# Kernel tuning notes

Hardware: AMD Instinct MI355X
Metric: run time of the kernel (lower is better)

The kernel has to match this reference:

```python
import jax, jax.numpy as jnp
import numpy as np

N_NODES = 30000
N_EDGES = 150000
N_REL = 10
IN_DIM = 256
OUT_DIM = 256


def setup_inputs() -> dict:
    key = jax.random.key(0)
    ks = jax.random.split(key, 10)
    s = 1.0 / np.sqrt(IN_DIM)  # ~nn.Linear init scale
    return {
        "x": jax.random.normal(ks[0], (N_NODES, IN_DIM), jnp.float32),
        "W_self": jax.random.uniform(ks[1], (IN_DIM, OUT_DIM), jnp.float32, -s, s),
        "b_self": jax.random.uniform(ks[2], (OUT_DIM,), jnp.float32, -s, s),
        "W_fwd": jax.random.uniform(ks[3], (N_REL, IN_DIM, OUT_DIM), jnp.float32, -s, s),
        "b_fwd": jax.random.uniform(ks[4], (N_REL, OUT_DIM), jnp.float32, -s, s),
        "W_rev": jax.random.uniform(ks[5], (N_REL, IN_DIM, OUT_DIM), jnp.float32, -s, s),
        "b_rev": jax.random.uniform(ks[6], (N_REL, OUT_DIM), jnp.float32, -s, s),
        "dep_idx": jax.random.randint(ks[7], (N_EDGES,), 0, N_NODES, jnp.int32),
        "rel_idx": jax.random.randint(ks[8], (N_EDGES,), 0, N_REL, jnp.int32),
        "gov_idx": jax.random.randint(ks[9], (N_EDGES,), 0, N_NODES, jnp.int32),
    }


def reference(x, W_self, b_self, W_fwd, b_fwd, W_rev, b_rev, dep_idx, rel_idx, gov_idx):
    # self transform for every token: [N, out]
    out = x @ W_self + b_self
    # transform all nodes by every relation weight up-front: [R, N, out]
    H_fwd = jnp.einsum("ni,rio->rno", x, W_fwd) + b_fwd[:, None, :]
    H_rev = jnp.einsum("ni,rio->rno", x, W_rev) + b_rev[:, None, :]
    # per-edge gather: forward msg uses governor feature, reverse msg uses dependent
    msg_fwd = H_fwd[rel_idx, gov_idx]  # [E, out]
    msg_rev = H_rev[rel_idx, dep_idx]  # [E, out]
    # scatter-add: forward msg -> dependent, reverse msg -> governor
    out = out.at[dep_idx].add(msg_fwd)
    out = out.at[gov_idx].add(msg_rev)
    return out
```

## Files before the change

### kernel.cpp

```cpp
#include <hip/hip_runtime.h>

#define N_NODES 30000
#define N_EDGES 150000
#define N_REL 10
#define DIM 256

#define SORT_BLOCKS 120
#define SORT_CHUNK ((N_EDGES + SORT_BLOCKS - 1) / SORT_BLOCKS)

#define SCAN_CHUNK 256
#define SCAN_BLOCKS ((N_NODES + SCAN_CHUNK - 1) / SCAN_CHUNK)

#define PREP_XB 7500
#define PREP_WB 5376

typedef __attribute__((ext_vector_type(8))) short bf16x8;
typedef __attribute__((ext_vector_type(4))) float f32x4;

__device__ __forceinline__ unsigned short f2bf(float f) {
  union { float f; unsigned int u; } v; v.f = f;
  unsigned int u = v.u;
  unsigned int r = u + 0x7fffu + ((u >> 16) & 1u);
  return (unsigned short)(r >> 16);
}


__global__ void prep_hist_kernel(const float* __restrict__ x,
                                 const float* __restrict__ Wf,
                                 const float* __restrict__ Wr,
                                 const float* __restrict__ Ws,
                                 const int* __restrict__ rel,
                                 const int* __restrict__ dep,
                                 const int* __restrict__ gov,
                                 unsigned short* __restrict__ xbf,
                                 unsigned short* __restrict__ wt,
                                 int* __restrict__ block_counts,
                                 int* __restrict__ cnt) {
  int b = blockIdx.x;
  if (b < PREP_XB) {
    int idx = b * 256 + threadIdx.x;
    float4 v = reinterpret_cast<const float4*>(x)[idx];
    ushort4 o;
    o.x = f2bf(v.x); o.y = f2bf(v.y); o.z = f2bf(v.z); o.w = f2bf(v.w);
    reinterpret_cast<ushort4*>(xbf)[idx] = o;
  } else if (b < PREP_XB + PREP_WB) {
    int idx = (b - PREP_XB) * 256 + threadIdx.x;
    int bb = idx >> 16;
    int t = idx & 65535;
    int o = t >> 8, i = t & 255;
    const float* src = (bb < N_REL) ? (Wf + (size_t)bb * 65536)
                     : (bb < 2 * N_REL) ? (Wr + (size_t)(bb - N_REL) * 65536)
                     : Ws;
    wt[idx] = f2bf(src[i * 256 + o]);
  } else {
    int hb = b - PREP_XB - PREP_WB;
    __shared__ int h[N_REL];
    if (threadIdx.x < N_REL) h[threadIdx.x] = 0;
    __syncthreads();
    int beg = hb * SORT_CHUNK;
    int end = min(beg + SORT_CHUNK, N_EDGES);
    for (int e = beg + threadIdx.x; e < end; e += blockDim.x) {
      atomicAdd(&h[rel[e]], 1);
      atomicAdd(&cnt[dep[e]], 1);
      atomicAdd(&cnt[N_NODES + gov[e]], 1);
    }
    __syncthreads();
    if (threadIdx.x < N_REL)
      block_counts[hb * N_REL + threadIdx.x] = h[threadIdx.x];
  }
}


__global__ void scanA_kernel(const int* __restrict__ cnt,
                             int* __restrict__ tmp, int* __restrict__ sums) {
  __shared__ int s[SCAN_CHUNK];
  int d = blockIdx.y, b = blockIdx.x, t = threadIdx.x;
  int i = b * SCAN_CHUNK + t;
  int v = (i < N_NODES) ? cnt[d * N_NODES + i] : 0;
  s[t] = v;
  __syncthreads();
  for (int off = 1; off < SCAN_CHUNK; off <<= 1) {
    int add = (t >= off) ? s[t - off] : 0;
    __syncthreads();
    s[t] += add;
    __syncthreads();
  }
  if (i < N_NODES) tmp[d * N_NODES + i] = s[t] - v;
  if (t == SCAN_CHUNK - 1) sums[d * SCAN_BLOCKS + b] = s[t];
}


__global__ void scan_finish_kernel(const int* __restrict__ sums,
                                   const int* __restrict__ tmp,
                                   const int* __restrict__ block_counts,
                                   int* __restrict__ rp,
                                   int* __restrict__ cursor,
                                   int* __restrict__ rel_start,
                                   int* __restrict__ block_offset) {
  int d = blockIdx.y, b = blockIdx.x, t = threadIdx.x;

  if (b == SCAN_BLOCKS) {
    if (d == 1) return;
    __shared__ int tot[N_REL];
    __shared__ int rstart[N_REL + 1];
    int r = t;
    if (r < N_REL) {
      int s = 0;
      for (int bb = 0; bb < SORT_BLOCKS; ++bb) s += block_counts[bb * N_REL + r];
      tot[r] = s;
    }
    __syncthreads();
    if (t == 0) {
      int s = 0;
      for (int i = 0; i < N_REL; ++i) { rstart[i] = s; s += tot[i]; }
      rstart[N_REL] = s;
      for (int i = 0; i <= N_REL; ++i) rel_start[i] = rstart[i];
    }
    __syncthreads();
    if (r < N_REL) {
      int run = rstart[r];
      for (int bb = 0; bb < SORT_BLOCKS; ++bb) {
        block_offset[bb * N_REL + r] = run;
        run += block_counts[bb * N_REL + r];
      }
    }
    return;
  }

  __shared__ int ssum[SCAN_BLOCKS];
  __shared__ int spre[SCAN_BLOCKS + 1];
  if (t < SCAN_BLOCKS) ssum[t] = sums[d * SCAN_BLOCKS + t];
  __syncthreads();
  if (t == 0) {
    int run = 0;
    for (int i = 0; i < SCAN_BLOCKS; ++i) { spre[i] = run; run += ssum[i]; }
    spre[SCAN_BLOCKS] = run;
  }
  __syncthreads();
  int chunk = spre[b];
  int i = b * SCAN_CHUNK + t;
  if (i < N_NODES) {
    int v = tmp[d * N_NODES + i] + chunk;
    rp[d * (N_NODES + 1) + i] = v;
    cursor[d * N_NODES + i] = v;
  }
  if (b == 0 && t == 0) rp[d * (N_NODES + 1) + N_NODES] = spre[SCAN_BLOCKS];
}


__global__ void scatter_all_kernel(const int* __restrict__ rel,
                                   const int* __restrict__ dep,
                                   const int* __restrict__ gov,
                                   const int* __restrict__ block_offset,
                                   int* __restrict__ cursor,
                                   int* __restrict__ perm,
                                   int* __restrict__ srcf,
                                   int* __restrict__ srcr,
                                   int* __restrict__ colf,
                                   int* __restrict__ colr) {
  __shared__ int cur[N_REL];
  if (threadIdx.x < N_REL)
    cur[threadIdx.x] = block_offset[blockIdx.x * N_REL + threadIdx.x];
  __syncthreads();
  int beg = blockIdx.x * SORT_CHUNK;
  int end = min(beg + SORT_CHUNK, N_EDGES);
  for (int e = beg + threadIdx.x; e < end; e += blockDim.x) {
    int dp = dep[e], gv = gov[e];
    int pos = atomicAdd(&cur[rel[e]], 1);
    perm[pos] = e;
    srcf[pos] = gv;
    srcr[pos] = dp;
    colf[atomicAdd(&cursor[dp], 1)] = pos;
    colr[atomicAdd(&cursor[N_NODES + gv], 1)] = pos;
  }
}


__global__ __launch_bounds__(256, 2)
void mega_gemm_kernel(const unsigned short* __restrict__ xbf,
                      const unsigned short* __restrict__ wt,
                      const float* __restrict__ b_self,
                      const float* __restrict__ b_fwd,
                      const float* __restrict__ b_rev,
                      const int* __restrict__ srcf,
                      const int* __restrict__ srcr,
                      const int* __restrict__ rel_start,
                      unsigned short* __restrict__ msg,
                      float* __restrict__ out) {
  const int bkt = blockIdx.y;
  const bool is_self = (bkt >= 2 * N_REL);
  const bool fwd = bkt < N_REL;
  const int r = is_self ? 0 : (fwd ? bkt : bkt - N_REL);

  int beg, cnt;
  const int* src_arr = fwd ? srcf : srcr;
  unsigned short* mdir = msg + (fwd ? 0 : (size_t)N_EDGES * DIM);
  if (is_self) {
    beg = (bkt - 2 * N_REL) * (N_NODES / 2);
    cnt = N_NODES / 2;
  } else {
    beg = rel_start[r];
    cnt = rel_start[r + 1] - beg;
  }
  const int ntiles = (cnt + 63) >> 6;
  const int GX = gridDim.x;

  const int tid = threadIdx.x;
  const int wave = tid >> 6, lane = tid & 63;
  const int lm = lane & 15, q = lane >> 4;
  const int nb = wave * 64;
  const int half = lane >> 5;

  __shared__ int s_src[2][64];
  __shared__ unsigned short sA[2][64 * DIM];

  bf16x8 wf[8][4];
  const unsigned short* wbase =
      wt + (size_t)(is_self ? 2 * N_REL : bkt) * DIM * DIM;
  #pragma unroll
  for (int kk = 0; kk < 8; ++kk)
    #pragma unroll
    for (int ni = 0; ni < 4; ++ni)
      wf[kk][ni] = *reinterpret_cast<const bf16x8*>(
          wbase + (size_t)(nb + ni * 16 + lm) * DIM + kk * 32 + q * 8);

  const float* bptr = is_self ? b_self : ((fwd ? b_fwd : b_rev) + r * DIM);
  float bias[4];
  #pragma unroll
  for (int ni = 0; ni < 4; ++ni) bias[ni] = bptr[nb + ni * 16 + lm];

  int swz[8];
  #pragma unroll
  for (int i = 0; i < 8; ++i)
    swz[i] = (((lane & 31) ^ ((i * 2 + half) & 7)) * 8);
  int rowoff[4];
  #pragma unroll
  for (int mi = 0; mi < 4; ++mi) rowoff[mi] = (mi * 16 + lm) * DIM;
  int ckoff[8];
  #pragma unroll
  for (int kk = 0; kk < 8; ++kk)
    ckoff[kk] = ((kk * 4 + q) ^ (lm & 7)) * 8;

  int t = blockIdx.x;
  if (t >= ntiles) return;

  auto load_idx = [&](int tt) -> int {
    int tile0_ = tt << 6;
    if (is_self) {
      int rr = beg + tile0_ + tid;
      return rr < beg + cnt ? rr : beg + cnt - 1;
    } else {
      int p_ = tile0_ + tid;
      p_ = p_ < cnt ? p_ : cnt - 1;
      return src_arr[beg + p_];
    }
  };

  auto issue_stage = [&](int p) {
    const int* sp = s_src[p];
    unsigned short* db = sA[p];
    #pragma unroll
    for (int i = 0; i < 8; ++i) {
      int ldsrow = wave * 16 + i * 2;
      int rr = sp[ldsrow + half];
      const unsigned short* g = xbf + (size_t)rr * DIM + swz[i];
      __builtin_amdgcn_global_load_lds(
          (const __attribute__((address_space(1))) void*)g,
          (__attribute__((address_space(3))) void*)(db + ldsrow * DIM),
          16, 0, 0);
    }
  };

  auto step = [&](int cur) {
    const int tile0 = t << 6;
    const int rows_valid = min(64, cnt - tile0);
    const bool have_next = (t + GX) < ntiles;
    const bool have_next2 = (t + 2 * GX) < ntiles;

    __syncthreads();
    if (have_next) issue_stage(cur ^ 1);
    if (tid < 64 && have_next2) s_src[cur][tid] = load_idx(t + 2 * GX);

    const unsigned short* sAb = sA[cur];
    #pragma unroll
    for (int mi = 0; mi < 4; ++mi) {
      bf16x8 a[8];
      #pragma unroll
      for (int kk = 0; kk < 8; ++kk)
        a[kk] = *reinterpret_cast<const bf16x8*>(sAb + rowoff[mi] + ckoff[kk]);

      f32x4 acc[4];
      #pragma unroll
      for (int ni = 0; ni < 4; ++ni) acc[ni] = (f32x4){0.f, 0.f, 0.f, 0.f};

      __builtin_amdgcn_s_setprio(1);
      #pragma unroll
      for (int kk = 0; kk < 8; ++kk)
        #pragma unroll
        for (int ni = 0; ni < 4; ++ni)
          acc[ni] = __builtin_amdgcn_mfma_f32_16x16x32_bf16(
              a[kk], wf[kk][ni], acc[ni], 0, 0, 0);
      __builtin_amdgcn_s_setprio(0);

      if (is_self) {
        #pragma unroll
        for (int reg = 0; reg < 4; ++reg) {
          int row = mi * 16 + q * 4 + reg;
          if (row < rows_valid) {
            #pragma unroll
            for (int ni = 0; ni < 4; ++ni)
              out[(size_t)(beg + tile0 + row) * DIM + nb + ni * 16 + lm] =
                  acc[ni][reg] + bias[ni];
          }
        }
      } else {
        #pragma unroll
        for (int reg = 0; reg < 4; ++reg) {
          int row = mi * 16 + q * 4 + reg;
          if (row < rows_valid) {
            unsigned long long p0 =
                ((unsigned long long)f2bf(acc[0][reg] + bias[0])) |
                ((unsigned long long)f2bf(acc[1][reg] + bias[1]) << 16) |
                ((unsigned long long)f2bf(acc[2][reg] + bias[2]) << 32) |
                ((unsigned long long)f2bf(acc[3][reg] + bias[3]) << 48);
            __builtin_nontemporal_store(
                p0, reinterpret_cast<unsigned long long*>(
                        mdir + (size_t)(beg + tile0 + row) * DIM + nb + lm * 4));
          }
        }
      }
    }
  };

  if (tid < 64) s_src[0][tid] = load_idx(t);
  __syncthreads();
  issue_stage(0);
  if (tid < 64 && t + GX < ntiles) s_src[1][tid] = load_idx(t + GX);

  while (true) {
    step(0);
    t += GX; if (t >= ntiles) break;
    step(1);
    t += GX; if (t >= ntiles) break;
  }
}


__global__ void reduce_both_kernel(const unsigned short* __restrict__ msg,
                                   const int* __restrict__ rp,
                                   const int* __restrict__ colf,
                                   const int* __restrict__ colr,
                                   float* __restrict__ out) {
  const int n = blockIdx.x * 4 + (threadIdx.x >> 6);
  if (n >= N_NODES) return;
  const int lane = threadIdx.x & 63;
  const int b0 = rp[n], e0 = rp[n + 1];
  const int b1 = rp[(N_NODES + 1) + n], e1 = rp[(N_NODES + 1) + n + 1];
  if (e0 == b0 && e1 == b1) return;

  float a0 = 0.f, a1 = 0.f, a2 = 0.f, a3 = 0.f;
  union { unsigned int u; float f; } c;

  auto accum = [&](unsigned long long v) {
    unsigned int lo = (unsigned int)v;
    unsigned int hi = (unsigned int)(v >> 32);
    c.u = lo << 16;          a0 += c.f;
    c.u = lo & 0xffff0000u;  a1 += c.f;
    c.u = hi << 16;          a2 += c.f;
    c.u = hi & 0xffff0000u;  a3 += c.f;
  };

  int j = b0;
  for (; j + 1 < e0; j += 2) {
    int r0 = colf[j], r1 = colf[j + 1];
    unsigned long long v0 = __builtin_nontemporal_load(
        reinterpret_cast<const unsigned long long*>(msg + (size_t)r0 * DIM + lane * 4));
    unsigned long long v1 = __builtin_nontemporal_load(
        reinterpret_cast<const unsigned long long*>(msg + (size_t)r1 * DIM + lane * 4));
    accum(v0); accum(v1);
  }
  if (j < e0) {
    unsigned long long v = __builtin_nontemporal_load(
        reinterpret_cast<const unsigned long long*>(msg + (size_t)colf[j] * DIM + lane * 4));
    accum(v);
  }
  const unsigned short* mrev = msg + (size_t)N_EDGES * DIM;
  j = b1;
  for (; j + 1 < e1; j += 2) {
    int r0 = colr[j], r1 = colr[j + 1];
    unsigned long long v0 = __builtin_nontemporal_load(
        reinterpret_cast<const unsigned long long*>(mrev + (size_t)r0 * DIM + lane * 4));
    unsigned long long v1 = __builtin_nontemporal_load(
        reinterpret_cast<const unsigned long long*>(mrev + (size_t)r1 * DIM + lane * 4));
    accum(v0); accum(v1);
  }
  if (j < e1) {
    unsigned long long v = __builtin_nontemporal_load(
        reinterpret_cast<const unsigned long long*>(mrev + (size_t)colr[j] * DIM + lane * 4));
    accum(v);
  }

  const int cb = (lane >> 4) * 64 + (lane & 15);
  float* op = out + (size_t)n * DIM;
  op[cb +  0] += a0;
  op[cb + 16] += a1;
  op[cb + 32] += a2;
  op[cb + 48] += a3;
}


__global__ __launch_bounds__(256, 2)
void self_gemm_kernel(const unsigned short* __restrict__ xbf,
                      const unsigned short* __restrict__ wt_self,
                      const float* __restrict__ b_self,
                      float* __restrict__ out) {
  const int tid = threadIdx.x;
  const int wave = tid >> 6, lane = tid & 63;
  const int lm = lane & 15, q = lane >> 4;
  const int nb = wave * 64;

  bf16x8 wf[8][4];
  #pragma unroll
  for (int kk = 0; kk < 8; ++kk)
    #pragma unroll
    for (int ni = 0; ni < 4; ++ni)
      wf[kk][ni] = *reinterpret_cast<const bf16x8*>(
          wt_self + (size_t)(nb + ni * 16 + lm) * DIM + kk * 32 + q * 8);

  float bias[4];
  #pragma unroll
  for (int ni = 0; ni < 4; ++ni) bias[ni] = b_self[nb + ni * 16 + lm];

  const int ntiles = (N_NODES + 63) / 64;
  for (int t = blockIdx.x; t < ntiles; t += gridDim.x) {
    const int row0 = t * 64;
    const unsigned short* xr[4];
    #pragma unroll
    for (int mi = 0; mi < 4; ++mi) {
      int r = row0 + mi * 16 + lm;
      int rc = r < N_NODES ? r : N_NODES - 1;
      xr[mi] = xbf + (size_t)rc * DIM + q * 8;
    }

    f32x4 acc[4][4];
    #pragma unroll
    for (int mi = 0; mi < 4; ++mi)
      #pragma unroll
      for (int ni = 0; ni < 4; ++ni)
        acc[mi][ni] = (f32x4){0.f, 0.f, 0.f, 0.f};

    #pragma unroll
    for (int kk = 0; kk < 8; ++kk) {
      bf16x8 a[4];
      #pragma unroll
      for (int mi = 0; mi < 4; ++mi)
        a[mi] = *reinterpret_cast<const bf16x8*>(xr[mi] + kk * 32);
      #pragma unroll
      for (int mi = 0; mi < 4; ++mi)
        #pragma unroll
        for (int ni = 0; ni < 4; ++ni)
          acc[mi][ni] = __builtin_amdgcn_mfma_f32_16x16x32_bf16(a[mi], wf[kk][ni], acc[mi][ni], 0, 0, 0);
    }

    #pragma unroll
    for (int mi = 0; mi < 4; ++mi) {
      #pragma unroll
      for (int reg = 0; reg < 4; ++reg) {
        int row = row0 + mi * 16 + q * 4 + reg;
        if (row < N_NODES) {
          #pragma unroll
          for (int ni = 0; ni < 4; ++ni)
            out[(size_t)row * DIM + nb + ni * 16 + lm] = acc[mi][ni][reg] + bias[ni];
        }
      }
    }
  }
}

__global__ void edge_gemm_atomic_kernel(const unsigned short* __restrict__ xbf,
                                        const unsigned short* __restrict__ wt,
                                        const float* __restrict__ b_fwd,
                                        const float* __restrict__ b_rev,
                                        const int* __restrict__ perm,
                                        const int* __restrict__ rel_start,
                                        const int* __restrict__ dep,
                                        const int* __restrict__ gov,
                                        float* __restrict__ out) {
  const int bucket = blockIdx.y;
  const int r = bucket % N_REL;
  const bool fwd = bucket < N_REL;
  const int beg = rel_start[r];
  const int cnt = rel_start[r + 1] - beg;
  const int ntiles = (cnt + 63) >> 6;

  const int tid = threadIdx.x;
  const int wave = tid >> 6, lane = tid & 63;
  const int lm = lane & 15, q = lane >> 4;
  const int nb = wave * 64;

  __shared__ int s_src[64], s_dst[64];

  const unsigned short* wr[4];
  #pragma unroll
  for (int ni = 0; ni < 4; ++ni)
    wr[ni] = wt + (size_t)bucket * DIM * DIM + (size_t)(nb + ni * 16 + lm) * DIM + q * 8;

  const float* bptr = (fwd ? b_fwd : b_rev) + r * DIM;
  float bias[4];
  #pragma unroll
  for (int ni = 0; ni < 4; ++ni) bias[ni] = bptr[nb + ni * 16 + lm];

  for (int t = blockIdx.x; t < ntiles; t += gridDim.x) {
    const int tile0 = t << 6;
    const int rows_valid = min(64, cnt - tile0);

    if (tid < 64) {
      int s = 0, d = -1;
      if (tid < rows_valid) {
        int e = perm[beg + tile0 + tid];
        int gv = gov[e], dp = dep[e];
        s = fwd ? gv : dp;
        d = fwd ? dp : gv;
      }
      s_src[tid] = s;
      s_dst[tid] = d;
    }
    __syncthreads();

    const unsigned short* xr[4];
    #pragma unroll
    for (int mi = 0; mi < 4; ++mi)
      xr[mi] = xbf + (size_t)s_src[mi * 16 + lm] * DIM + q * 8;

    f32x4 acc[4][4];
    #pragma unroll
    for (int mi = 0; mi < 4; ++mi)
      #pragma unroll
      for (int ni = 0; ni < 4; ++ni)
        acc[mi][ni] = (f32x4){0.f, 0.f, 0.f, 0.f};

    #pragma unroll
    for (int k0 = 0; k0 < DIM; k0 += 32) {
      bf16x8 a[4], b[4];
      #pragma unroll
      for (int mi = 0; mi < 4; ++mi) a[mi] = *reinterpret_cast<const bf16x8*>(xr[mi] + k0);
      #pragma unroll
      for (int ni = 0; ni < 4; ++ni) b[ni] = *reinterpret_cast<const bf16x8*>(wr[ni] + k0);
      #pragma unroll
      for (int mi = 0; mi < 4; ++mi)
        #pragma unroll
        for (int ni = 0; ni < 4; ++ni)
          acc[mi][ni] = __builtin_amdgcn_mfma_f32_16x16x32_bf16(a[mi], b[ni], acc[mi][ni], 0, 0, 0);
    }

    #pragma unroll
    for (int mi = 0; mi < 4; ++mi) {
      #pragma unroll
      for (int reg = 0; reg < 4; ++reg) {
        int row = mi * 16 + q * 4 + reg;
        if (row < rows_valid) {
          int dst = s_dst[row];
          float* op = out + (size_t)dst * DIM + nb + lm;
          #pragma unroll
          for (int ni = 0; ni < 4; ++ni)
            atomicAdd(op + ni * 16, acc[mi][ni][reg] + bias[ni]);
        }
      }
    }
    __syncthreads();
  }
}


extern "C" void kernel_launch(void* const* d_in, const int* in_sizes, int n_in,
                              void* d_out, int out_size, void* d_ws, size_t ws_size,
                              hipStream_t stream) {
  const float* x      = (const float*)d_in[0];
  const float* W_self = (const float*)d_in[1];
  const float* b_self = (const float*)d_in[2];
  const float* W_fwd  = (const float*)d_in[3];
  const float* b_fwd  = (const float*)d_in[4];
  const float* W_rev  = (const float*)d_in[5];
  const float* b_rev  = (const float*)d_in[6];
  const int* dep = (const int*)d_in[7];
  const int* rel = (const int*)d_in[8];
  const int* gov = (const int*)d_in[9];
  float* out = (float*)d_out;

  char* base = (char*)d_ws;
  size_t off = 0;
  auto alloc = [&](size_t bytes) -> char* {
    char* p = base + off;
    off = (off + bytes + 15) & ~(size_t)15;
    return p;
  };

  unsigned short* xbf = (unsigned short*)alloc((size_t)N_NODES * DIM * 2);
  unsigned short* wt  = (unsigned short*)alloc((size_t)21 * DIM * DIM * 2);
  int* perm          = (int*)alloc((size_t)N_EDGES * 4);
  int* srcf          = (int*)alloc((size_t)N_EDGES * 4);
  int* srcr          = (int*)alloc((size_t)N_EDGES * 4);
  int* rel_start     = (int*)alloc(16 * 4);
  int* block_counts  = (int*)alloc(SORT_BLOCKS * N_REL * 4);
  int* block_offset  = (int*)alloc(SORT_BLOCKS * N_REL * 4);
  int* cnt       = (int*)alloc((size_t)2 * N_NODES * 4);
  int* tmp       = (int*)alloc((size_t)2 * N_NODES * 4);
  int* sums      = (int*)alloc((size_t)2 * SCAN_BLOCKS * 4);
  int* rp        = (int*)alloc((size_t)2 * (N_NODES + 1) * 4);
  int* cursor    = (int*)alloc((size_t)2 * N_NODES * 4);
  int* colf      = (int*)alloc((size_t)N_EDGES * 4);
  int* colr      = (int*)alloc((size_t)N_EDGES * 4);
  unsigned short* msg = (unsigned short*)alloc((size_t)2 * N_EDGES * DIM * 2);
  const bool two_phase = (off <= ws_size);

  hipMemsetAsync(cnt, 0, (size_t)2 * N_NODES * 4, stream);
  prep_hist_kernel<<<PREP_XB + PREP_WB + SORT_BLOCKS, 256, 0, stream>>>(
      x, W_fwd, W_rev, W_self, rel, dep, gov, xbf, wt, block_counts, cnt);
  scanA_kernel<<<dim3(SCAN_BLOCKS, 2), SCAN_CHUNK, 0, stream>>>(cnt, tmp, sums);
  scan_finish_kernel<<<dim3(SCAN_BLOCKS + 1, 2), SCAN_CHUNK, 0, stream>>>(
      sums, tmp, block_counts, rp, cursor, rel_start, block_offset);
  scatter_all_kernel<<<SORT_BLOCKS, 256, 0, stream>>>(
      rel, dep, gov, block_offset, cursor, perm, srcf, srcr, colf, colr);

  if (two_phase) {
    mega_gemm_kernel<<<dim3(48, 2 * N_REL + 2), 256, 0, stream>>>(
        xbf, wt, b_self, b_fwd, b_rev, srcf, srcr, rel_start, msg, out);
    reduce_both_kernel<<<(N_NODES + 3) / 4, 256, 0, stream>>>(
        msg, rp, colf, colr, out);
  } else {
    self_gemm_kernel<<<120, 256, 0, stream>>>(
        xbf, wt + (size_t)20 * DIM * DIM, b_self, out);
    edge_gemm_atomic_kernel<<<dim3(260, 20), 256, 0, stream>>>(
        xbf, wt, b_fwd, b_rev, perm, rel_start, dep, gov, out);
  }
}
```

Baseline: 277.1 us.

## Write edge messages directly in destination-CSR order to make reduce contiguous

The GEMM epilogue now scatters each message row to its CSR position, taken from per-edge position arrays computed in the scatter kernel, instead of writing it in relation-sorted order. The reduce kernel can then read contiguous message rows per node without the colf/colr indirection. This trades coalesced contiguous stores in the GEMM (now scattered 512-byte rows, no longer nontemporal) for contiguous loads and one fewer dependent index load in the reduce.

```diff
diff --git a/kernel.cpp b/kernel.cpp
--- a/kernel.cpp
+++ b/kernel.cpp
@@ -156,8 +156,8 @@
                                    int* __restrict__ perm,
                                    int* __restrict__ srcf,
                                    int* __restrict__ srcr,
-                                   int* __restrict__ colf,
-                                   int* __restrict__ colr) {
+                                   int* __restrict__ posf,
+                                   int* __restrict__ posr) {
   __shared__ int cur[N_REL];
   if (threadIdx.x < N_REL)
     cur[threadIdx.x] = block_offset[blockIdx.x * N_REL + threadIdx.x];
@@ -170,8 +170,8 @@
     perm[pos] = e;
     srcf[pos] = gv;
     srcr[pos] = dp;
-    colf[atomicAdd(&cursor[dp], 1)] = pos;
-    colr[atomicAdd(&cursor[N_NODES + gv], 1)] = pos;
+    posf[pos] = atomicAdd(&cursor[dp], 1);
+    posr[pos] = atomicAdd(&cursor[N_NODES + gv], 1);
   }
 }
 
@@ -184,6 +184,8 @@
                       const float* __restrict__ b_rev,
                       const int* __restrict__ srcf,
                       const int* __restrict__ srcr,
+                      const int* __restrict__ posf,
+                      const int* __restrict__ posr,
                       const int* __restrict__ rel_start,
                       unsigned short* __restrict__ msg,
                       float* __restrict__ out) {
@@ -194,6 +196,7 @@
 
   int beg, cnt;
   const int* src_arr = fwd ? srcf : srcr;
+  const int* pos_arr = fwd ? posf : posr;
   unsigned short* mdir = msg + (fwd ? 0 : (size_t)N_EDGES * DIM);
   if (is_self) {
     beg = (bkt - 2 * N_REL) * (N_NODES / 2);
@@ -280,6 +283,15 @@
     __syncthreads();
     if (have_next) issue_stage(cur ^ 1);
     if (tid < 64 && have_next2) s_src[cur][tid] = load_idx(t + 2 * GX);
+
+    int pos_s[4][4];
+    if (!is_self) {
+      #pragma unroll
+      for (int mi = 0; mi < 4; ++mi)
+        #pragma unroll
+        for (int reg = 0; reg < 4; ++reg)
+          pos_s[mi][reg] = pos_arr[beg + tile0 + mi * 16 + q * 4 + reg];
+    }
 
     const unsigned short* sAb = sA[cur];
     #pragma unroll
@@ -318,14 +330,13 @@
         for (int reg = 0; reg < 4; ++reg) {
           int row = mi * 16 + q * 4 + reg;
           if (row < rows_valid) {
-            unsigned long long p0 =
-                ((unsigned long long)f2bf(acc[0][reg] + bias[0])) |
-                ((unsigned long long)f2bf(acc[1][reg] + bias[1]) << 16) |
-                ((unsigned long long)f2bf(acc[2][reg] + bias[2]) << 32) |
-                ((unsigned long long)f2bf(acc[3][reg] + bias[3]) << 48);
-            __builtin_nontemporal_store(
-                p0, reinterpret_cast<unsigned long long*>(
-                        mdir + (size_t)(beg + tile0 + row) * DIM + nb + lm * 4));
+            unsigned int p0 = ((unsigned int)f2bf(acc[1][reg] + bias[1]) << 16) |
+                              f2bf(acc[0][reg] + bias[0]);
+            unsigned int p1 = ((unsigned int)f2bf(acc[3][reg] + bias[3]) << 16) |
+                              f2bf(acc[2][reg] + bias[2]);
+            uint2 u; u.x = p0; u.y = p1;
+            *reinterpret_cast<uint2*>(
+                mdir + (size_t)pos_s[mi][reg] * DIM + nb + lm * 4) = u;
           }
         }
       }
@@ -348,8 +359,6 @@
 
 __global__ void reduce_both_kernel(const unsigned short* __restrict__ msg,
                                    const int* __restrict__ rp,
-                                   const int* __restrict__ colf,
-                                   const int* __restrict__ colr,
                                    float* __restrict__ out) {
   const int n = blockIdx.x * 4 + (threadIdx.x >> 6);
   if (n >= N_NODES) return;
@@ -372,31 +381,29 @@
 
   int j = b0;
   for (; j + 1 < e0; j += 2) {
-    int r0 = colf[j], r1 = colf[j + 1];
     unsigned long long v0 = __builtin_nontemporal_load(
-        reinterpret_cast<const unsigned long long*>(msg + (size_t)r0 * DIM + lane * 4));
+        reinterpret_cast<const unsigned long long*>(msg + (size_t)j * DIM + lane * 4));
     unsigned long long v1 = __builtin_nontemporal_load(
-        reinterpret_cast<const unsigned long long*>(msg + (size_t)r1 * DIM + lane * 4));
+        reinterpret_cast<const unsigned long long*>(msg + (size_t)(j + 1) * DIM + lane * 4));
     accum(v0); accum(v1);
   }
   if (j < e0) {
     unsigned long long v = __builtin_nontemporal_load(
-        reinterpret_cast<const unsigned long long*>(msg + (size_t)colf[j] * DIM + lane * 4));
+        reinterpret_cast<const unsigned long long*>(msg + (size_t)j * DIM + lane * 4));
     accum(v);
   }
   const unsigned short* mrev = msg + (size_t)N_EDGES * DIM;
   j = b1;
   for (; j + 1 < e1; j += 2) {
-    int r0 = colr[j], r1 = colr[j + 1];
     unsigned long long v0 = __builtin_nontemporal_load(
-        reinterpret_cast<const unsigned long long*>(mrev + (size_t)r0 * DIM + lane * 4));
+        reinterpret_cast<const unsigned long long*>(mrev + (size_t)j * DIM + lane * 4));
     unsigned long long v1 = __builtin_nontemporal_load(
-        reinterpret_cast<const unsigned long long*>(mrev + (size_t)r1 * DIM + lane * 4));
+        reinterpret_cast<const unsigned long long*>(mrev + (size_t)(j + 1) * DIM + lane * 4));
     accum(v0); accum(v1);
   }
   if (j < e1) {
     unsigned long long v = __builtin_nontemporal_load(
-        reinterpret_cast<const unsigned long long*>(mrev + (size_t)colr[j] * DIM + lane * 4));
+        reinterpret_cast<const unsigned long long*>(mrev + (size_t)j * DIM + lane * 4));
     accum(v);
   }
 
@@ -600,6 +607,8 @@
   int* perm          = (int*)alloc((size_t)N_EDGES * 4);
   int* srcf          = (int*)alloc((size_t)N_EDGES * 4);
   int* srcr          = (int*)alloc((size_t)N_EDGES * 4);
+  int* posf          = (int*)alloc((size_t)(N_EDGES + 64) * 4);
+  int* posr          = (int*)alloc((size_t)(N_EDGES + 64) * 4);
   int* rel_start     = (int*)alloc(16 * 4);
   int* block_counts  = (int*)alloc(SORT_BLOCKS * N_REL * 4);
   int* block_offset  = (int*)alloc(SORT_BLOCKS * N_REL * 4);
@@ -608,8 +617,6 @@
   int* sums      = (int*)alloc((size_t)2 * SCAN_BLOCKS * 4);
   int* rp        = (int*)alloc((size_t)2 * (N_NODES + 1) * 4);
   int* cursor    = (int*)alloc((size_t)2 * N_NODES * 4);
-  int* colf      = (int*)alloc((size_t)N_EDGES * 4);
-  int* colr      = (int*)alloc((size_t)N_EDGES * 4);
   unsigned short* msg = (unsigned short*)alloc((size_t)2 * N_EDGES * DIM * 2);
   const bool two_phase = (off <= ws_size);
 
@@ -620,13 +627,12 @@
   scan_finish_kernel<<<dim3(SCAN_BLOCKS + 1, 2), SCAN_CHUNK, 0, stream>>>(
       sums, tmp, block_counts, rp, cursor, rel_start, block_offset);
   scatter_all_kernel<<<SORT_BLOCKS, 256, 0, stream>>>(
-      rel, dep, gov, block_offset, cursor, perm, srcf, srcr, colf, colr);
+      rel, dep, gov, block_offset, cursor, perm, srcf, srcr, posf, posr);
 
   if (two_phase) {
     mega_gemm_kernel<<<dim3(48, 2 * N_REL + 2), 256, 0, stream>>>(
-        xbf, wt, b_self, b_fwd, b_rev, srcf, srcr, rel_start, msg, out);
-    reduce_both_kernel<<<(N_NODES + 3) / 4, 256, 0, stream>>>(
-        msg, rp, colf, colr, out);
+        xbf, wt, b_self, b_fwd, b_rev, srcf, srcr, posf, posr, rel_start, msg, out);
+    reduce_both_kernel<<<(N_NODES + 3) / 4, 256, 0, stream>>>(msg, rp, out);
   } else {
     self_gemm_kernel<<<120, 256, 0, stream>>>(
         xbf, wt + (size_t)20 * DIM * DIM, b_self, out);
```

After: 273.4 us. About the same (-1.3%).
